# Kernel tuning notes

Hardware: AMD Instinct MI355X
Metric: run time of the kernel (lower is better)

The kernel has to match this reference:

```python
import jax, jax.numpy as jnp
import numpy as np

B, H, N, D = 4, 16, 1024, 64


def setup_inputs() -> dict:
    key = jax.random.key(0)
    ks = jax.random.split(key, 6)
    return {
        "q": jax.random.normal(ks[0], (B, H, N, D), dtype=jnp.float32),
        "k": jax.random.normal(ks[1], (B, H, N, D), dtype=jnp.float32),
        "v": jax.random.normal(ks[2], (B, H, N, D), dtype=jnp.float32),
        "attn_bias": jax.random.normal(ks[3], (H, N, N), dtype=jnp.float32),
        # 1x1 Conv2d over head channel == h->h matrix (PyTorch default init scale)
        "w_pre": jax.random.normal(ks[4], (H, H), dtype=jnp.float32) * (1.0 / np.sqrt(H)),
        "w_post": jax.random.normal(ks[5], (H, H), dtype=jnp.float32) * (1.0 / np.sqrt(H)),
    }


def reference(q, k, v, attn_bias, w_pre, w_post):
    # Attend.forward with causal=True, talking_heads=True, dropout=0 (eval),
    # mask=None, prev_attn=None, scale=None -> d**-0.5, qk_norm=False -> fp32 softmax.
    scale = q.shape[-1] ** -0.5
    dots = jnp.einsum('bhid,bhjd->bhij', q, k) * scale          # [b,h,i,j]
    # pre-softmax talking heads: 1x1 conv over head channel
    dots = jnp.einsum('gh,bhij->bgij', w_pre, dots)
    dots = dots + attn_bias                                     # [h,i,j] broadcasts
    n = dots.shape[-1]
    causal_mask = jnp.triu(jnp.ones((n, n), dtype=bool), 1)
    mask_value = -jnp.finfo(dots.dtype).max
    dots = jnp.where(causal_mask, mask_value, dots)
    attn = jax.nn.softmax(dots.astype(jnp.float32), axis=-1).astype(dots.dtype)
    # post-softmax talking heads
    attn = jnp.einsum('gh,bhij->bgij', w_post, attn)
    out = jnp.einsum('bhij,bhjd->bhid', attn, v)                # [b,h,i,d]
    return out
```

## Files before the change

### kernel.cpp

```cpp
#include <hip/hip_runtime.h>
#include <math.h>


#define NB 4
#define NH 16
#define NS 1024
#define ND 64
#define IT 16
#define JT 64
#define NITEM 544
#define HPAD 24
#define PERB_E ((size_t)NITEM * 64 * 256)

typedef __bf16 bf16x8 __attribute__((ext_vector_type(8)));
typedef __bf16 bf16x4 __attribute__((ext_vector_type(4)));
typedef float  f32x4  __attribute__((ext_vector_type(4)));

__device__ __forceinline__ f32x4 fzero4() {
  f32x4 z; z[0] = 0.f; z[1] = 0.f; z[2] = 0.f; z[3] = 0.f; return z;
}

__device__ __forceinline__ void lgkm_barrier() {
  asm volatile("s_waitcnt lgkmcnt(0)" ::: "memory");
  __builtin_amdgcn_s_barrier();
}

__device__ __forceinline__ void decode_item(int q, int& i0, int& j0) {
  int m = (int)sqrtf((float)q * 0.5f) + 1;
  while (2 * m * (m + 1) > q) --m;
  while (2 * (m + 1) * (m + 2) <= q) ++m;
  const int off = q - 2 * m * (m + 1);
  const int t = off / (m + 1);
  const int c = off - t * (m + 1);
  i0 = (4 * m + t) * IT;
  j0 = JT * c;
}

__device__ __forceinline__ size_t ebase64(int r) {
  const int m = r >> 2, t = r & 3;
  return (size_t)(r + 2 * m * (m - 1) + t * m);
}

#define QK_BLKS 8192
#define VT_BLKS 1024
#define BT_BLKS 4096

__global__ __launch_bounds__(256)
void prep(const float* __restrict__ Q, const float* __restrict__ K,
          const float* __restrict__ V, const float* __restrict__ Bg,
          __bf16* __restrict__ Qb, __bf16* __restrict__ Kb,
          __bf16* __restrict__ VT, __bf16* __restrict__ BT, int doBT) {
  __shared__ float tile[64][65];
  __shared__ float tmp[16][257];
  const int bid = blockIdx.x;
  const int t = threadIdx.x;
  if (bid < QK_BLKS) {
    const size_t nq4 = (size_t)NB * NH * NS * ND / 4;
    size_t idx = (size_t)bid * 256 + t;
    if (idx < nq4) {
      float4 x = reinterpret_cast<const float4*>(Q)[idx];
      bf16x4 o;
      o[0] = (__bf16)(x.x * 0.125f); o[1] = (__bf16)(x.y * 0.125f);
      o[2] = (__bf16)(x.z * 0.125f); o[3] = (__bf16)(x.w * 0.125f);
      reinterpret_cast<bf16x4*>(Qb)[idx] = o;
    } else {
      idx -= nq4;
      float4 x = reinterpret_cast<const float4*>(K)[idx];
      bf16x4 o;
      o[0] = (__bf16)x.x; o[1] = (__bf16)x.y; o[2] = (__bf16)x.z; o[3] = (__bf16)x.w;
      reinterpret_cast<bf16x4*>(Kb)[idx] = o;
    }
  } else if (bid < QK_BLKS + VT_BLKS) {
    const int vb = bid - QK_BLKS;
    const int bh = vb >> 4;
    const int j0 = (vb & 15) * 64;
    const float* vp = V + ((size_t)bh * NS + j0) * ND;
#pragma unroll
    for (int rep = 0; rep < 4; ++rep) {
      int lin = rep * 256 + t;
      int jj = lin >> 4;
      int dd = (lin & 15) * 4;
      float4 x = *reinterpret_cast<const float4*>(vp + (size_t)jj * ND + dd);
      tile[jj][dd] = x.x; tile[jj][dd + 1] = x.y;
      tile[jj][dd + 2] = x.z; tile[jj][dd + 3] = x.w;
    }
    __syncthreads();
    __bf16* op = VT + (size_t)bh * ND * NS + j0;
#pragma unroll
    for (int rep = 0; rep < 16; ++rep) {
      int lin = rep * 256 + t;
      int d = lin >> 6;
      int jj = lin & 63;
      op[(size_t)d * NS + jj] = (__bf16)tile[jj][d];
    }
  } else if (doBT) {
    const int tb = bid - QK_BLKS - VT_BLKS;
    const int i = tb >> 2;
    const int j0 = (tb & 3) * 256;
    if (j0 > i) return;
#pragma unroll
    for (int g = 0; g < NH; ++g)
      tmp[g][t] = Bg[(size_t)g * NS * NS + (size_t)i * NS + j0 + t];
    __syncthreads();
    __bf16* op = BT + ((size_t)i * NS + j0) * NH;
#pragma unroll
    for (int rep = 0; rep < 16; ++rep) {
      const int j = rep * 16 + (t >> 4);
      const int g = t & 15;
      op[(size_t)(rep * 256 + t)] = (__bf16)tmp[g][j];
    }
  }
}

template <bool QKWS, bool BTWS>
__global__ __launch_bounds__(512, 2)
void attend_e(const float* __restrict__ Qg, const float* __restrict__ Kg,
              const float* __restrict__ Bg, const float* __restrict__ Wpre,
              const __bf16* __restrict__ Qb, const __bf16* __restrict__ Kb,
              const __bf16* __restrict__ BT,
              __bf16* __restrict__ Ews, float* __restrict__ Lws)
{
  const int bid = blockIdx.x;
  const int b = bid / NITEM;
  int i0, jlo;
  decode_item(NITEM - 1 - (bid - b * NITEM), i0, jlo);
  const int r = i0 >> 4;
  const int jmax = ((r >> 2) + 1) * JT;
  __bf16* Eb = Ews + (size_t)b * PERB_E + ebase64(r) * 64 * 256;

  const int tid = threadIdx.x;
  const int w = tid >> 6;
  const int lane = tid & 63;
  const int lr = lane & 15;
  const int lg = lane >> 4;

  __shared__ __align__(16) __bf16 dots[IT * JT * HPAD];

  bf16x8 kreg[2][4][2];
#pragma unroll
  for (int hh = 0; hh < 2; ++hh) {
    const int h = w + hh * 8;
#pragma unroll
    for (int jb = 0; jb < 4; ++jb)
#pragma unroll
      for (int ks = 0; ks < 2; ++ks) {
        if constexpr (QKWS) {
          kreg[hh][jb][ks] = *reinterpret_cast<const bf16x8*>(
              Kb + ((size_t)(b * NH + h) * NS + jlo + jb * 16 + lr) * ND + ks * 32 + lg * 8);
        } else {
          const float* kp = Kg + ((size_t)(b * NH + h) * NS + jlo + jb * 16 + lr) * ND + ks * 32 + lg * 8;
          float4 x = *reinterpret_cast<const float4*>(kp);
          float4 y = *reinterpret_cast<const float4*>(kp + 4);
          bf16x8 f;
          f[0] = (__bf16)x.x; f[1] = (__bf16)x.y; f[2] = (__bf16)x.z; f[3] = (__bf16)x.w;
          f[4] = (__bf16)y.x; f[5] = (__bf16)y.y; f[6] = (__bf16)y.z; f[7] = (__bf16)y.w;
          kreg[hh][jb][ks] = f;
        }
      }
  }
  bf16x8 qF[2][2];
#pragma unroll
  for (int hh = 0; hh < 2; ++hh) {
    const int h = w + hh * 8;
    if constexpr (QKWS) {
      const __bf16* qp = Qb + ((size_t)(b * NH + h) * NS + i0 + lr) * ND + lg * 8;
      qF[hh][0] = *reinterpret_cast<const bf16x8*>(qp);
      qF[hh][1] = *reinterpret_cast<const bf16x8*>(qp + 32);
    } else {
      const float* qp = Qg + ((size_t)(b * NH + h) * NS + i0 + lr) * ND + lg * 8;
#pragma unroll
      for (int ks = 0; ks < 2; ++ks) {
        float4 x = *reinterpret_cast<const float4*>(qp + ks * 32);
        float4 y = *reinterpret_cast<const float4*>(qp + ks * 32 + 4);
        bf16x8 f;
        f[0] = (__bf16)(x.x * 0.125f); f[1] = (__bf16)(x.y * 0.125f);
        f[2] = (__bf16)(x.z * 0.125f); f[3] = (__bf16)(x.w * 0.125f);
        f[4] = (__bf16)(y.x * 0.125f); f[5] = (__bf16)(y.y * 0.125f);
        f[6] = (__bf16)(y.z * 0.125f); f[7] = (__bf16)(y.w * 0.125f);
        qF[hh][ks] = f;
      }
    }
  }
  bf16x4 braw[2][4];
  float brf[2][4][4];
#pragma unroll
  for (int ii = 0; ii < 2; ++ii) {
    const int gi = i0 + w + ii * 8;
#pragma unroll
    for (int qq = 0; qq < 4; ++qq) {
      if constexpr (BTWS) {
        braw[ii][qq] = *reinterpret_cast<const bf16x4*>(
            BT + ((size_t)gi * NS + jlo + qq * 16 + lr) * NH + lg * 4);
      } else {
#pragma unroll
        for (int rr = 0; rr < 4; ++rr)
          brf[ii][qq][rr] = Bg[((size_t)(lg * 4 + rr) * NS + gi) * NS + jlo + qq * 16 + lr];
      }
    }
  }
  bf16x8 wpreF;
#pragma unroll
  for (int e = 0; e < 8; ++e) wpreF[e] = (__bf16)0.f;
  if (lg < 2) {
#pragma unroll
    for (int e = 0; e < 8; ++e) wpreF[e] = (__bf16)Wpre[lr * NH + lg * 8 + e];
  }

#pragma unroll
  for (int hh = 0; hh < 2; ++hh) {
    const int h = w + hh * 8;
#pragma unroll
    for (int jb = 0; jb < 4; ++jb) {
      f32x4 acc = fzero4();
#pragma unroll
      for (int ks = 0; ks < 2; ++ks)
        acc = __builtin_amdgcn_mfma_f32_16x16x32_bf16(qF[hh][ks], kreg[hh][jb][ks], acc, 0, 0, 0);
#pragma unroll
      for (int rr = 0; rr < 4; ++rr)
        dots[((lg * 4 + rr) * JT + jb * 16 + lr) * HPAD + h] = (__bf16)acc[rr];
    }
  }
  lgkm_barrier();

  float Lp[2][4];
#pragma unroll
  for (int ii = 0; ii < 2; ++ii)
#pragma unroll
    for (int rr = 0; rr < 4; ++rr) Lp[ii][rr] = 0.f;

#pragma unroll
  for (int ii = 0; ii < 2; ++ii) {
    const int i = w + ii * 8;
    const int gi = i0 + i;
#pragma unroll
    for (int qq = 0; qq < 4; ++qq) {
      bf16x8 bfr;
#pragma unroll
      for (int e = 0; e < 8; ++e) bfr[e] = (__bf16)0.f;
      if (lg < 2)
        bfr = *reinterpret_cast<const bf16x8*>(&dots[(i * JT + qq * 16 + lr) * HPAD + lg * 8]);
      f32x4 s1 = __builtin_amdgcn_mfma_f32_16x16x32_bf16(wpreF, bfr, fzero4(), 0, 0, 0);
      const int gj = jlo + qq * 16 + lr;
      bf16x4 epack;
#pragma unroll
      for (int rr = 0; rr < 4; ++rr) {
        float bv;
        if constexpr (BTWS) bv = (float)braw[ii][qq][rr];
        else                bv = brf[ii][qq][rr];
        float ev = 0.f;
        if (gj <= gi) ev = __expf(s1[rr] + bv);
        Lp[ii][rr] += ev;
        epack[rr] = (__bf16)ev;
      }
      *reinterpret_cast<bf16x4*>(Eb + ((size_t)i * jmax + gj) * 16 + lg * 4) = epack;
    }
  }

#pragma unroll
  for (int ii = 0; ii < 2; ++ii)
#pragma unroll
    for (int rr = 0; rr < 4; ++rr) {
      float v = Lp[ii][rr];
      v += __shfl_xor(v, 1, 64);
      v += __shfl_xor(v, 2, 64);
      v += __shfl_xor(v, 4, 64);
      v += __shfl_xor(v, 8, 64);
      if (lr == 0)
        atomicAdd(&Lws[(size_t)(b * NH + lg * 4 + rr) * NS + i0 + w + ii * 8], v);
    }
}

template <bool VWS>
__global__ __launch_bounds__(1024)
void attend_pv(const float* __restrict__ Vg, const float* __restrict__ Wpost,
               const __bf16* __restrict__ VTb, const __bf16* __restrict__ Ews,
               const float* __restrict__ Lws, float* __restrict__ Og)
{
  const int bid = blockIdx.x;
  const int x = bid & 7;
  const int q = bid >> 3;
  const int b = x >> 1;
  const int r = 63 - (q * 2 + (x & 1));
  const int i0 = r * IT;
  const int nsteps = (r >> 2) + 1;
  const int jmax = nsteps * JT;
  const __bf16* Eb = Ews + (size_t)b * PERB_E + ebase64(r) * 64 * 256;

  const int tid = threadIdx.x;
  const int w = tid >> 6;
  const int lane = tid & 63;
  const int lr = lane & 15;
  const int lg = lane >> 4;

  __shared__ __align__(16) __bf16 sbP2[2][256 * 64];

  bf16x8 wpostF;
#pragma unroll
  for (int e = 0; e < 8; ++e) wpostF[e] = (__bf16)0.f;
  if (lg < 2) {
#pragma unroll
    for (int e = 0; e < 8; ++e) {
      const int h = lg * 8 + e;
      const float L = Lws[(size_t)(b * NH + h) * NS + i0 + w];
      wpostF[e] = (__bf16)(Wpost[lr * NH + h] / L);
    }
  }

  f32x4 oacc[4];
#pragma unroll
  for (int db = 0; db < 4; ++db) oacc[db] = fzero4();

  bf16x8 eA[4], eB[4];
  bf16x8 vA[2], vB[2];

  auto load_e = [&](bf16x8 (&buf)[4], int j0) {
#pragma unroll
    for (int qq = 0; qq < 4; ++qq) {
#pragma unroll
      for (int e = 0; e < 8; ++e) buf[qq][e] = (__bf16)0.f;
      if (lg < 2)
        buf[qq] = *reinterpret_cast<const bf16x8*>(
            Eb + ((size_t)w * jmax + j0 + qq * 16 + lr) * 16 + lg * 8);
    }
  };
  auto load_v = [&](bf16x8 (&buf)[2], int j0, int db) {
    if constexpr (VWS) {
      const __bf16* vp = VTb + ((size_t)(b * NH + w) * ND + db * 16 + lr) * NS + j0 + lg * 8;
      buf[0] = *reinterpret_cast<const bf16x8*>(vp);
      buf[1] = *reinterpret_cast<const bf16x8*>(vp + 32);
    } else {
      const float* vp = Vg + (size_t)(b * NH + w) * NS * ND;
      bf16x8 f0, f1;
#pragma unroll
      for (int e = 0; e < 8; ++e) {
        f0[e] = (__bf16)vp[(size_t)(j0 + lg * 8 + e) * ND + db * 16 + lr];
        f1[e] = (__bf16)vp[(size_t)(j0 + 32 + lg * 8 + e) * ND + db * 16 + lr];
      }
      buf[0] = f0; buf[1] = f1;
    }
  };

  auto do_step = [&](int s, bf16x8 (&ecur)[4], bf16x8 (&enxt)[4]) {
    const int cur = s & 1;
    const int j0 = s * JT;
    load_v(vA, j0, 0);
    load_v(vB, j0, 1);
    if (s + 1 < nsteps) load_e(enxt, j0 + JT);
#pragma unroll
    for (int qq = 0; qq < 4; ++qq) {
      f32x4 p2 = __builtin_amdgcn_mfma_f32_16x16x32_bf16(wpostF, ecur[qq], fzero4(), 0, 0, 0);
      const int u = (qq * 16 + lr) >> 3;
#pragma unroll
      for (int rr = 0; rr < 4; ++rr) {
        const int row = (lg * 4 + rr) * IT + w;
        sbP2[cur][row * 64 + ((u ^ (w & 7)) << 3) + (lr & 7)] = (__bf16)p2[rr];
      }
    }
    lgkm_barrier();
    const int row = w * IT + lr;
    const int sw = lr & 7;
    bf16x8 pf0 = *reinterpret_cast<const bf16x8*>(&sbP2[cur][row * 64 + ((lg ^ sw) << 3)]);
    bf16x8 pf1 = *reinterpret_cast<const bf16x8*>(&sbP2[cur][row * 64 + (((4 + lg) ^ sw) << 3)]);
    oacc[0] = __builtin_amdgcn_mfma_f32_16x16x32_bf16(pf0, vA[0], oacc[0], 0, 0, 0);
    oacc[0] = __builtin_amdgcn_mfma_f32_16x16x32_bf16(pf1, vA[1], oacc[0], 0, 0, 0);
    load_v(vA, j0, 2);
    oacc[1] = __builtin_amdgcn_mfma_f32_16x16x32_bf16(pf0, vB[0], oacc[1], 0, 0, 0);
    oacc[1] = __builtin_amdgcn_mfma_f32_16x16x32_bf16(pf1, vB[1], oacc[1], 0, 0, 0);
    load_v(vB, j0, 3);
    oacc[2] = __builtin_amdgcn_mfma_f32_16x16x32_bf16(pf0, vA[0], oacc[2], 0, 0, 0);
    oacc[2] = __builtin_amdgcn_mfma_f32_16x16x32_bf16(pf1, vA[1], oacc[2], 0, 0, 0);
    oacc[3] = __builtin_amdgcn_mfma_f32_16x16x32_bf16(pf0, vB[0], oacc[3], 0, 0, 0);
    oacc[3] = __builtin_amdgcn_mfma_f32_16x16x32_bf16(pf1, vB[1], oacc[3], 0, 0, 0);
  };

  load_e(eA, 0);
  for (int s = 0; s < nsteps; s += 2) {
    do_step(s, eA, eB);
    if (s + 1 < nsteps) do_step(s + 1, eB, eA);
  }

  float* ob = Og + ((size_t)(b * NH + w) * NS + i0) * ND;
#pragma unroll
  for (int db = 0; db < 4; ++db)
#pragma unroll
    for (int rr = 0; rr < 4; ++rr)
      ob[(size_t)(lg * 4 + rr) * ND + db * 16 + lr] = oacc[db][rr];
}

extern "C" void kernel_launch(void* const* d_in, const int* in_sizes, int n_in,
                              void* d_out, int out_size, void* d_ws, size_t ws_size,
                              hipStream_t stream) {
  const float* Q     = (const float*)d_in[0];
  const float* K     = (const float*)d_in[1];
  const float* V     = (const float*)d_in[2];
  const float* BIAS  = (const float*)d_in[3];
  const float* WPRE  = (const float*)d_in[4];
  const float* WPOST = (const float*)d_in[5];
  float* OUT = (float*)d_out;
  (void)in_sizes; (void)n_in; (void)out_size;

  const size_t nelem    = (size_t)NB * NH * NS * ND;
  const size_t E_BYTES  = (size_t)NB * PERB_E * 2;
  const size_t off_E    = 1u << 20;
  const size_t off_VT   = off_E + E_BYTES;
  const size_t off_Qb   = off_VT + nelem * 2;
  const size_t off_Kb   = off_Qb + nelem * 2;
  const size_t off_BT   = off_Kb + nelem * 2;
  const size_t BT_BYTES = (size_t)NS * NS * NH * 2;
  const size_t need_full = off_BT + BT_BYTES;
  const size_t need_A    = off_BT;
  const size_t need_C    = off_VT;

  float* Lws = (float*)d_ws;
  hipMemsetAsync(d_ws, 0, (size_t)NB * NH * NS * sizeof(float), stream);

  const int grid_e = NB * NITEM;
  if (ws_size >= need_C) {
    __bf16* Ews = (__bf16*)((char*)d_ws + off_E);
    if (ws_size >= need_full) {
      __bf16* VT = (__bf16*)((char*)d_ws + off_VT);
      __bf16* Qb = (__bf16*)((char*)d_ws + off_Qb);
      __bf16* Kb = (__bf16*)((char*)d_ws + off_Kb);
      __bf16* BT = (__bf16*)((char*)d_ws + off_BT);
      hipLaunchKernelGGL(prep, dim3(QK_BLKS + VT_BLKS + BT_BLKS), dim3(256), 0, stream,
                         Q, K, V, BIAS, Qb, Kb, VT, BT, 1);
      hipLaunchKernelGGL((attend_e<true, true>), dim3(grid_e), dim3(512), 0, stream,
                         Q, K, BIAS, WPRE, Qb, Kb, BT, Ews, Lws);
      hipLaunchKernelGGL((attend_pv<true>), dim3(NB * 64), dim3(1024), 0, stream,
                         V, WPOST, VT, Ews, Lws, OUT);
    } else if (ws_size >= need_A) {
      __bf16* VT = (__bf16*)((char*)d_ws + off_VT);
      __bf16* Qb = (__bf16*)((char*)d_ws + off_Qb);
      __bf16* Kb = (__bf16*)((char*)d_ws + off_Kb);
      hipLaunchKernelGGL(prep, dim3(QK_BLKS + VT_BLKS), dim3(256), 0, stream,
                         Q, K, V, BIAS, Qb, Kb, VT, (__bf16*)nullptr, 0);
      hipLaunchKernelGGL((attend_e<true, false>), dim3(grid_e), dim3(512), 0, stream,
                         Q, K, BIAS, WPRE, Qb, Kb, (const __bf16*)nullptr, Ews, Lws);
      hipLaunchKernelGGL((attend_pv<true>), dim3(NB * 64), dim3(1024), 0, stream,
                         V, WPOST, VT, Ews, Lws, OUT);
    } else {
      hipLaunchKernelGGL((attend_e<false, false>), dim3(grid_e), dim3(512), 0, stream,
                         Q, K, BIAS, WPRE, (const __bf16*)nullptr, (const __bf16*)nullptr,
                         (const __bf16*)nullptr, Ews, Lws);
      hipLaunchKernelGGL((attend_pv<false>), dim3(NB * 64), dim3(1024), 0, stream,
                         V, WPOST, (const __bf16*)nullptr, Ews, Lws, OUT);
    }
  } else {
    __bf16* Ews = (__bf16*)((char*)d_ws + off_E);
    hipLaunchKernelGGL((attend_e<false, false>), dim3(grid_e), dim3(512), 0, stream,
                       Q, K, BIAS, WPRE, (const __bf16*)nullptr, (const __bf16*)nullptr,
                       (const __bf16*)nullptr, Ews, Lws);
    hipLaunchKernelGGL((attend_pv<false>), dim3(NB * 64), dim3(1024), 0, stream,
                       V, WPOST, (const __bf16*)nullptr, Ews, Lws, OUT);
  }
}
```

Before: 191.5 us.

## Process two attention tiles per block with prefetched loads for the second

Each attend_e block now handles two work items (pairing item k with item k+272, interleaved across batches via bid&3), halving the grid. Loads for the second tile are issued before the first tile's softmax/exp phase so memory latency overlaps compute, and the batch mapping changes to round-robin. This costs more registers for the double set of K/Q/bias fragments, which may reduce occupancy or cause spills, plus two extra barriers.

New measurement: 208.7 us. 1.09x slower.

```diff
diff --git a/kernel.cpp b/kernel.cpp
--- a/kernel.cpp
+++ b/kernel.cpp
@@ -121,12 +121,11 @@
               __bf16* __restrict__ Ews, float* __restrict__ Lws)
 {
   const int bid = blockIdx.x;
-  const int b = bid / NITEM;
-  int i0, jlo;
-  decode_item(NITEM - 1 - (bid - b * NITEM), i0, jlo);
-  const int r = i0 >> 4;
-  const int jmax = ((r >> 2) + 1) * JT;
-  __bf16* Eb = Ews + (size_t)b * PERB_E + ebase64(r) * 64 * 256;
+  const int b = bid & 3;
+  const int localA = bid >> 2;
+  int i0A, jloA, i0B, jloB;
+  decode_item(NITEM - 1 - localA, i0A, jloA);
+  decode_item(NITEM - 1 - (localA + 272), i0B, jloB);
 
   const int tid = threadIdx.x;
   const int w = tid >> 6;
@@ -136,68 +135,6 @@
 
   __shared__ __align__(16) __bf16 dots[IT * JT * HPAD];
 
-  bf16x8 kreg[2][4][2];
-#pragma unroll
-  for (int hh = 0; hh < 2; ++hh) {
-    const int h = w + hh * 8;
-#pragma unroll
-    for (int jb = 0; jb < 4; ++jb)
-#pragma unroll
-      for (int ks = 0; ks < 2; ++ks) {
-        if constexpr (QKWS) {
-          kreg[hh][jb][ks] = *reinterpret_cast<const bf16x8*>(
-              Kb + ((size_t)(b * NH + h) * NS + jlo + jb * 16 + lr) * ND + ks * 32 + lg * 8);
-        } else {
-          const float* kp = Kg + ((size_t)(b * NH + h) * NS + jlo + jb * 16 + lr) * ND + ks * 32 + lg * 8;
-          float4 x = *reinterpret_cast<const float4*>(kp);
-          float4 y = *reinterpret_cast<const float4*>(kp + 4);
-          bf16x8 f;
-          f[0] = (__bf16)x.x; f[1] = (__bf16)x.y; f[2] = (__bf16)x.z; f[3] = (__bf16)x.w;
-          f[4] = (__bf16)y.x; f[5] = (__bf16)y.y; f[6] = (__bf16)y.z; f[7] = (__bf16)y.w;
-          kreg[hh][jb][ks] = f;
-        }
-      }
-  }
-  bf16x8 qF[2][2];
-#pragma unroll
-  for (int hh = 0; hh < 2; ++hh) {
-    const int h = w + hh * 8;
-    if constexpr (QKWS) {
-      const __bf16* qp = Qb + ((size_t)(b * NH + h) * NS + i0 + lr) * ND + lg * 8;
-      qF[hh][0] = *reinterpret_cast<const bf16x8*>(qp);
-      qF[hh][1] = *reinterpret_cast<const bf16x8*>(qp + 32);
-    } else {
-      const float* qp = Qg + ((size_t)(b * NH + h) * NS + i0 + lr) * ND + lg * 8;
-#pragma unroll
-      for (int ks = 0; ks < 2; ++ks) {
-        float4 x = *reinterpret_cast<const float4*>(qp + ks * 32);
-        float4 y = *reinterpret_cast<const float4*>(qp + ks * 32 + 4);
-        bf16x8 f;
-        f[0] = (__bf16)(x.x * 0.125f); f[1] = (__bf16)(x.y * 0.125f);
-        f[2] = (__bf16)(x.z * 0.125f); f[3] = (__bf16)(x.w * 0.125f);
-        f[4] = (__bf16)(y.x * 0.125f); f[5] = (__bf16)(y.y * 0.125f);
-        f[6] = (__bf16)(y.z * 0.125f); f[7] = (__bf16)(y.w * 0.125f);
-        qF[hh][ks] = f;
-      }
-    }
-  }
-  bf16x4 braw[2][4];
-  float brf[2][4][4];
-#pragma unroll
-  for (int ii = 0; ii < 2; ++ii) {
-    const int gi = i0 + w + ii * 8;
-#pragma unroll
-    for (int qq = 0; qq < 4; ++qq) {
-      if constexpr (BTWS) {
-        braw[ii][qq] = *reinterpret_cast<const bf16x4*>(
-            BT + ((size_t)gi * NS + jlo + qq * 16 + lr) * NH + lg * 4);
-      } else {
-#pragma unroll
-        for (int rr = 0; rr < 4; ++rr)
-          brf[ii][qq][rr] = Bg[((size_t)(lg * 4 + rr) * NS + gi) * NS + jlo + qq * 16 + lr];
-      }
-    }
-  }
   bf16x8 wpreF;
 #pragma unroll
   for (int e = 0; e < 8; ++e) wpreF[e] = (__bf16)0.f;
@@ -206,68 +143,149 @@
     for (int e = 0; e < 8; ++e) wpreF[e] = (__bf16)Wpre[lr * NH + lg * 8 + e];
   }
 
-#pragma unroll
-  for (int hh = 0; hh < 2; ++hh) {
-    const int h = w + hh * 8;
-#pragma unroll
-    for (int jb = 0; jb < 4; ++jb) {
-      f32x4 acc = fzero4();
-#pragma unroll
-      for (int ks = 0; ks < 2; ++ks)
-        acc = __builtin_amdgcn_mfma_f32_16x16x32_bf16(qF[hh][ks], kreg[hh][jb][ks], acc, 0, 0, 0);
-#pragma unroll
-      for (int rr = 0; rr < 4; ++rr)
-        dots[((lg * 4 + rr) * JT + jb * 16 + lr) * HPAD + h] = (__bf16)acc[rr];
-    }
-  }
+  bf16x8 kA[2][4][2], kB[2][4][2];
+  bf16x8 qAF[2][2], qBF[2][2];
+  bf16x4 baA[2][4], baB[2][4];
+  float  bfA[2][4][4], bfB[2][4][4];
+
+  auto stage = [&](int i0, int jlo, bf16x8 (&kreg)[2][4][2], bf16x8 (&qF)[2][2],
+                   bf16x4 (&braw)[2][4], float (&brf)[2][4][4]) {
+#pragma unroll
+    for (int hh = 0; hh < 2; ++hh) {
+      const int h = w + hh * 8;
+#pragma unroll
+      for (int jb = 0; jb < 4; ++jb)
+#pragma unroll
+        for (int ks = 0; ks < 2; ++ks) {
+          if constexpr (QKWS) {
+            kreg[hh][jb][ks] = *reinterpret_cast<const bf16x8*>(
+                Kb + ((size_t)(b * NH + h) * NS + jlo + jb * 16 + lr) * ND + ks * 32 + lg * 8);
+          } else {
+            const float* kp = Kg + ((size_t)(b * NH + h) * NS + jlo + jb * 16 + lr) * ND + ks * 32 + lg * 8;
+            float4 x = *reinterpret_cast<const float4*>(kp);
+            float4 y = *reinterpret_cast<const float4*>(kp + 4);
+            bf16x8 f;
+            f[0] = (__bf16)x.x; f[1] = (__bf16)x.y; f[2] = (__bf16)x.z; f[3] = (__bf16)x.w;
+            f[4] = (__bf16)y.x; f[5] = (__bf16)y.y; f[6] = (__bf16)y.z; f[7] = (__bf16)y.w;
+            kreg[hh][jb][ks] = f;
+          }
+        }
+    }
+#pragma unroll
+    for (int hh = 0; hh < 2; ++hh) {
+      const int h = w + hh * 8;
+      if constexpr (QKWS) {
+        const __bf16* qp = Qb + ((size_t)(b * NH + h) * NS + i0 + lr) * ND + lg * 8;
+        qF[hh][0] = *reinterpret_cast<const bf16x8*>(qp);
+        qF[hh][1] = *reinterpret_cast<const bf16x8*>(qp + 32);
+      } else {
+        const float* qp = Qg + ((size_t)(b * NH + h) * NS + i0 + lr) * ND + lg * 8;
+#pragma unroll
+        for (int ks = 0; ks < 2; ++ks) {
+          float4 x = *reinterpret_cast<const float4*>(qp + ks * 32);
+          float4 y = *reinterpret_cast<const float4*>(qp + ks * 32 + 4);
+          bf16x8 f;
+          f[0] = (__bf16)(x.x * 0.125f); f[1] = (__bf16)(x.y * 0.125f);
+          f[2] = (__bf16)(x.z * 0.125f); f[3] = (__bf16)(x.w * 0.125f);
+          f[4] = (__bf16)(y.x * 0.125f); f[5] = (__bf16)(y.y * 0.125f);
+          f[6] = (__bf16)(y.z * 0.125f); f[7] = (__bf16)(y.w * 0.125f);
+          qF[hh][ks] = f;
+        }
+      }
+    }
+#pragma unroll
+    for (int ii = 0; ii < 2; ++ii) {
+      const int gi = i0 + w + ii * 8;
+#pragma unroll
+      for (int qq = 0; qq < 4; ++qq) {
+        if constexpr (BTWS) {
+          braw[ii][qq] = *reinterpret_cast<const bf16x4*>(
+              BT + ((size_t)gi * NS + jlo + qq * 16 + lr) * NH + lg * 4);
+        } else {
+#pragma unroll
+          for (int rr = 0; rr < 4; ++rr)
+            brf[ii][qq][rr] = Bg[((size_t)(lg * 4 + rr) * NS + gi) * NS + jlo + qq * 16 + lr];
+        }
+      }
+    }
+  };
+
+  auto qk = [&](bf16x8 (&kreg)[2][4][2], bf16x8 (&qF)[2][2]) {
+#pragma unroll
+    for (int hh = 0; hh < 2; ++hh) {
+      const int h = w + hh * 8;
+#pragma unroll
+      for (int jb = 0; jb < 4; ++jb) {
+        f32x4 acc = fzero4();
+#pragma unroll
+        for (int ks = 0; ks < 2; ++ks)
+          acc = __builtin_amdgcn_mfma_f32_16x16x32_bf16(qF[hh][ks], kreg[hh][jb][ks], acc, 0, 0, 0);
+#pragma unroll
+        for (int rr = 0; rr < 4; ++rr)
+          dots[((lg * 4 + rr) * JT + jb * 16 + lr) * HPAD + h] = (__bf16)acc[rr];
+      }
+    }
+  };
+
+  auto phase2 = [&](int i0, int jlo, bf16x4 (&braw)[2][4], float (&brf)[2][4][4]) {
+    const int r = i0 >> 4;
+    const int jmax = ((r >> 2) + 1) * JT;
+    __bf16* Eb = Ews + (size_t)b * PERB_E + ebase64(r) * 64 * 256;
+    float Lp[2][4];
+#pragma unroll
+    for (int ii = 0; ii < 2; ++ii)
+#pragma unroll
+      for (int rr = 0; rr < 4; ++rr) Lp[ii][rr] = 0.f;
+#pragma unroll
+    for (int ii = 0; ii < 2; ++ii) {
+      const int i = w + ii * 8;
+      const int gi = i0 + i;
+#pragma unroll
+      for (int qq = 0; qq < 4; ++qq) {
+        bf16x8 bfr;
+#pragma unroll
+        for (int e = 0; e < 8; ++e) bfr[e] = (__bf16)0.f;
+        if (lg < 2)
+          bfr = *reinterpret_cast<const bf16x8*>(&dots[(i * JT + qq * 16 + lr) * HPAD + lg * 8]);
+        f32x4 s1 = __builtin_amdgcn_mfma_f32_16x16x32_bf16(wpreF, bfr, fzero4(), 0, 0, 0);
+        const int gj = jlo + qq * 16 + lr;
+        bf16x4 epack;
+#pragma unroll
+        for (int rr = 0; rr < 4; ++rr) {
+          float bv;
+          if constexpr (BTWS) bv = (float)braw[ii][qq][rr];
+          else                bv = brf[ii][qq][rr];
+          float ev = 0.f;
+          if (gj <= gi) ev = __expf(s1[rr] + bv);
+          Lp[ii][rr] += ev;
+          epack[rr] = (__bf16)ev;
+        }
+        *reinterpret_cast<bf16x4*>(Eb + ((size_t)i * jmax + gj) * 16 + lg * 4) = epack;
+      }
+    }
+#pragma unroll
+    for (int ii = 0; ii < 2; ++ii)
+#pragma unroll
+      for (int rr = 0; rr < 4; ++rr) {
+        float v = Lp[ii][rr];
+        v += __shfl_xor(v, 1, 64);
+        v += __shfl_xor(v, 2, 64);
+        v += __shfl_xor(v, 4, 64);
+        v += __shfl_xor(v, 8, 64);
+        if (lr == 0)
+          atomicAdd(&Lws[(size_t)(b * NH + lg * 4 + rr) * NS + i0 + w + ii * 8], v);
+      }
+  };
+
+  stage(i0A, jloA, kA, qAF, baA, bfA);
+  qk(kA, qAF);
+  stage(i0B, jloB, kB, qBF, baB, bfB);
   lgkm_barrier();
-
-  float Lp[2][4];
-#pragma unroll
-  for (int ii = 0; ii < 2; ++ii)
-#pragma unroll
-    for (int rr = 0; rr < 4; ++rr) Lp[ii][rr] = 0.f;
-
-#pragma unroll
-  for (int ii = 0; ii < 2; ++ii) {
-    const int i = w + ii * 8;
-    const int gi = i0 + i;
-#pragma unroll
-    for (int qq = 0; qq < 4; ++qq) {
-      bf16x8 bfr;
-#pragma unroll
-      for (int e = 0; e < 8; ++e) bfr[e] = (__bf16)0.f;
-      if (lg < 2)
-        bfr = *reinterpret_cast<const bf16x8*>(&dots[(i * JT + qq * 16 + lr) * HPAD + lg * 8]);
-      f32x4 s1 = __builtin_amdgcn_mfma_f32_16x16x32_bf16(wpreF, bfr, fzero4(), 0, 0, 0);
-      const int gj = jlo + qq * 16 + lr;
-      bf16x4 epack;
-#pragma unroll
-      for (int rr = 0; rr < 4; ++rr) {
-        float bv;
-        if constexpr (BTWS) bv = (float)braw[ii][qq][rr];
-        else                bv = brf[ii][qq][rr];
-        float ev = 0.f;
-        if (gj <= gi) ev = __expf(s1[rr] + bv);
-        Lp[ii][rr] += ev;
-        epack[rr] = (__bf16)ev;
-      }
-      *reinterpret_cast<bf16x4*>(Eb + ((size_t)i * jmax + gj) * 16 + lg * 4) = epack;
-    }
-  }
-
-#pragma unroll
-  for (int ii = 0; ii < 2; ++ii)
-#pragma unroll
-    for (int rr = 0; rr < 4; ++rr) {
-      float v = Lp[ii][rr];
-      v += __shfl_xor(v, 1, 64);
-      v += __shfl_xor(v, 2, 64);
-      v += __shfl_xor(v, 4, 64);
-      v += __shfl_xor(v, 8, 64);
-      if (lr == 0)
-        atomicAdd(&Lws[(size_t)(b * NH + lg * 4 + rr) * NS + i0 + w + ii * 8], v);
-    }
+  phase2(i0A, jloA, baA, bfA);
+  lgkm_barrier();
+  qk(kB, qBF);
+  lgkm_barrier();
+  phase2(i0B, jloB, baB, bfB);
 }
 
 template <bool VWS>
@@ -414,7 +432,7 @@
   float* Lws = (float*)d_ws;
   hipMemsetAsync(d_ws, 0, (size_t)NB * NH * NS * sizeof(float), stream);
 
-  const int grid_e = NB * NITEM;
+  const int grid_e = NB * NITEM / 2;
   if (ws_size >= need_C) {
     __bf16* Ews = (__bf16*)((char*)d_ws + off_E);
     if (ws_size >= need_full) {
```
